# Optimization experiments

Hardware: AMD Instinct MI355X
Metric: run time of the kernel (lower is better)

## Reference

```python
import jax, jax.numpy as jnp
import numpy as np

N, E, C, NS, NB, NH = 20000, 320000, 64, 4, 8, 64
AVG_NEIGH = 16.0

def setup_inputs() -> dict:
    key = jax.random.key(0)
    ks = jax.random.split(key, 16)
    inp = {}
    inp['vectors'] = 0.35 * jax.random.normal(ks[0], (E, 3), jnp.float32)
    inp['node_scalars'] = jax.random.normal(ks[1], (N, C), jnp.float32)
    inp['node_vectors'] = jax.random.normal(ks[2], (N, C, 3), jnp.float32)
    inp['node_specie'] = jax.random.randint(ks[3], (N,), 0, NS)
    inp['senders'] = jax.random.randint(ks[4], (E,), 0, N)
    inp['receivers'] = jax.random.randint(ks[5], (E,), 0, N)
    # indexed skip linear: node irreps (64x0e+64x1o) -> 64x0e+64x1o+64x0e (scalars incl. gates)
    inp['W_skip_s'] = jax.random.normal(ks[6], (NS, C, 2 * C), jnp.float32) / np.sqrt(C)
    inp['W_skip_v'] = jax.random.normal(ks[7], (NS, C, C), jnp.float32) / np.sqrt(C)
    inp['W_up_s'] = jax.random.normal(ks[8], (C, C), jnp.float32) / np.sqrt(C)
    inp['W_up_v'] = jax.random.normal(ks[9], (C, C), jnp.float32) / np.sqrt(C)
    inp['W_mlp0'] = jax.random.normal(ks[10], (NB, NH), jnp.float32) / np.sqrt(NB)
    inp['W_mlp1'] = jax.random.normal(ks[11], (NH, NH), jnp.float32) / np.sqrt(NH)
    inp['W_mlp2'] = jax.random.normal(ks[12], (NH, 4 * C), jnp.float32) / np.sqrt(NH)
    inp['W_down_s'] = jax.random.normal(ks[13], (2 * C, 2 * C), jnp.float32) / np.sqrt(2 * C)
    inp['W_down_v'] = jax.random.normal(ks[14], (2 * C, C), jnp.float32) / np.sqrt(2 * C)
    return inp


def _forward(vectors, node_scalars, node_vectors, node_specie, senders, receivers,
             W_skip_s, W_skip_v, W_up_s, W_up_v, W_mlp0, W_mlp1, W_mlp2, W_down_s, W_down_v):
    n = node_scalars.shape[0]
    # --- self connection (specie-indexed linear) ---
    skip_s = jnp.einsum('ni,nio->no', node_scalars, W_skip_s[node_specie])   # [N,128]
    skip_v = jnp.einsum('nim,nio->nom', node_vectors, W_skip_v[node_specie]) # [N,64,3]
    # --- linear up ---
    s = node_scalars @ W_up_s                                  # [N,64]
    v = jnp.einsum('nim,io->nom', node_vectors, W_up_v)        # [N,64,3]
    ms, mv = s[senders], v[senders]                            # gather -> [E,64], [E,64,3]
    # --- spherical harmonics l=1, component normalization (|Y|=sqrt(3)) ---
    lengths = jnp.linalg.norm(vectors, axis=1, keepdims=True)  # [E,1]
    vhat = vectors / jnp.where(lengths == 0.0, 1.0, lengths)
    Y = jnp.sqrt(3.0) * vhat                                   # [E,3]
    # --- tensor product, filter_ir_out = {0e,1o} ---
    t1 = ms[:, :, None] * Y[:, None, :]                        # 0e x 1o -> 1o [E,64,3]
    t0 = jnp.einsum('ecm,em->ec', mv, Y) / jnp.sqrt(3.0)       # 1o x 1o -> 0e [E,64]
    msg_s = jnp.concatenate([ms, t0], axis=1)                  # [E,128]
    msg_v = jnp.concatenate([mv, t1], axis=1)                  # [E,128,3]
    # --- radial basis * polynomial envelope -> MLP ---
    x = lengths[:, 0]
    nvec = jnp.arange(1, NB + 1, dtype=vectors.dtype)
    safe_x = jnp.where(x == 0.0, 1.0, x)
    bess = jnp.sqrt(2.0) * jnp.sin(nvec * jnp.pi * x[:, None]) / safe_x[:, None]  # [E,8]
    u = jnp.clip(x, 0.0, 1.0)
    env = jnp.where(x < 1.0, 1.0 - 28.0 * u**6 + 48.0 * u**7 - 21.0 * u**8, 0.0)  # poly_envelope(5,2)
    h = jax.nn.swish((bess * env[:, None]) @ W_mlp0)
    h = jax.nn.swish(h @ W_mlp1)
    mix = h @ W_mlp2                                           # [E,256] = 128x0e + 128x1o weights
    mix = jnp.where(lengths == 0.0, 0.0, mix)
    msg_s = msg_s * mix[:, : 2 * C]
    msg_v = msg_v * mix[:, 2 * C :, None]
    # --- scatter-add to receivers, normalize by sqrt(avg_num_neighbors) ---
    inv = 1.0 / jnp.sqrt(AVG_NEIGH)
    agg_s = jnp.zeros((n, 2 * C), msg_s.dtype).at[receivers].add(msg_s) * inv
    agg_v = jnp.zeros((n, 2 * C, 3), msg_v.dtype).at[receivers].add(msg_v) * inv
    # --- linear down to 64x0e + 64x1o + 64x0e(gates) ---
    out_s = agg_s @ W_down_s + skip_s                          # [N,128]
    out_v = jnp.einsum('nim,io->nom', agg_v, W_down_v) + skip_v  # [N,64,3]
    # --- gate: swish on scalars, swish(gates) modulates vectors ---
    scal = jax.nn.swish(out_s[:, :C])
    gates = jax.nn.swish(out_s[:, C:])
    vec = out_v * gates[:, :, None]
    return jnp.concatenate([scal, vec.reshape(n, 3 * C)], axis=1)  # [N,256]


def reference(vectors, node_scalars, node_vectors, node_specie, senders, receivers,
              W_skip_s, W_skip_v, W_up_s, W_up_v, W_mlp0, W_mlp1, W_mlp2, W_down_s, W_down_v):
    return _forward(vectors, node_scalars, node_vectors, node_specie, senders, receivers,
                    W_skip_s, W_skip_v, W_up_s, W_up_v, W_mlp0, W_mlp1, W_mlp2, W_down_s, W_down_v)
```

## Files before the change

### kernel.cpp

```cpp
#include <hip/hip_runtime.h>
#include <math.h>

#define PI_F        3.14159265358979323846f
#define SQRT2_F     1.41421356237309515f
#define SQRT3_F     1.73205080756887729f
#define INV_SQRT3_F 0.57735026918962576f
#define INV_AVG     0.25f

#define N_NODES 20000
#define N_EDGES 320000

__device__ __forceinline__ float swish_f(float x) {
    return x / (1.f + __expf(-x));
}

__global__ __launch_bounds__(256) void k_zero_cnt(int* __restrict__ cnt) {
    const int i = blockIdx.x * 256 + threadIdx.x;
    if (i < N_NODES) cnt[i] = 0;
}
__global__ __launch_bounds__(256) void k_hist(const int* __restrict__ rcv,
                                              int* __restrict__ cnt) {
    const int e = blockIdx.x * 256 + threadIdx.x;
    if (e < N_EDGES) atomicAdd(&cnt[rcv[e]], 1);
}
__global__ __launch_bounds__(1024) void k_scan(const int* __restrict__ cnt,
                                               int* __restrict__ cursor) {
    __shared__ int part[1024];
    const int t = threadIdx.x;
    const int base = t * 20;
    int s = 0;
    #pragma unroll
    for (int j = 0; j < 20; ++j) {
        const int idx = base + j;
        if (idx < N_NODES) s += cnt[idx];
    }
    part[t] = s;
    __syncthreads();
    for (int d = 1; d < 1024; d <<= 1) {
        const int v = (t >= d) ? part[t - d] : 0;
        __syncthreads();
        part[t] += v;
        __syncthreads();
    }
    int run = (t == 0) ? 0 : part[t - 1];
    for (int j = 0; j < 20; ++j) {
        const int idx = base + j;
        if (idx < N_NODES) { cursor[idx] = run; run += cnt[idx]; }
    }
}
__global__ __launch_bounds__(256) void k_scatter(const int* __restrict__ rcv,
                                                 int* __restrict__ cursor,
                                                 int* __restrict__ perm) {
    const int e = blockIdx.x * 256 + threadIdx.x;
    if (e < N_EDGES) {
        const int pos = atomicAdd(&cursor[rcv[e]], 1);
        perm[pos] = e;
    }
}

__global__ __launch_bounds__(256) void k_node_up(
    const float* __restrict__ ns, const float* __restrict__ nv,
    const float* __restrict__ Wus, const float* __restrict__ Wuv,
    float* __restrict__ s_up, float* __restrict__ v_up,
    float* __restrict__ agg_s, float* __restrict__ agg_v)
{
    const int lane = threadIdx.x & 63;
    const int wq   = __builtin_amdgcn_readfirstlane(threadIdx.x >> 6);
    const int n    = blockIdx.x * 4 + wq;

    const float* nsr = ns + n * 64;
    const float* nvr = nv + n * 192;
    float acc = 0.f, a0 = 0.f, a1 = 0.f, a2 = 0.f;
    for (int i = 0; i < 64; ++i) {
        const float s = nsr[i];
        acc = fmaf(s, Wus[i*64 + lane], acc);
        const float wv = Wuv[i*64 + lane];
        a0 = fmaf(nvr[i*3+0], wv, a0);
        a1 = fmaf(nvr[i*3+1], wv, a1);
        a2 = fmaf(nvr[i*3+2], wv, a2);
    }
    s_up[n*64 + lane] = acc;
    v_up[(n*64 + lane)*3 + 0] = a0;
    v_up[(n*64 + lane)*3 + 1] = a1;
    v_up[(n*64 + lane)*3 + 2] = a2;

    agg_s[n*128 + lane]      = 0.f;
    agg_s[n*128 + 64 + lane] = 0.f;
    #pragma unroll
    for (int k = 0; k < 6; ++k) agg_v[n*384 + k*64 + lane] = 0.f;
}

__global__ __launch_bounds__(256, 4) void k_edge(
    const float* __restrict__ vecs,
    const int*   __restrict__ snd_idx, const int* __restrict__ rcv_idx,
    const int*   __restrict__ perm,
    const float* __restrict__ W0, const float* __restrict__ W1,
    const float* __restrict__ W2,
    const float* __restrict__ s_up, const float* __restrict__ v_up,
    float* __restrict__ agg_s, float* __restrict__ agg_v)
{
    __shared__ float h1v[64*69];
    __shared__ float h2v[64*69];

    const int tid  = threadIdx.x;
    const int lane = tid & 63;
    const int wq   = __builtin_amdgcn_readfirstlane(tid >> 6);
    const int e0   = blockIdx.x * 64;
    const int c    = lane & 15, q = lane >> 4;

    const int pe_l  = perm[e0 + lane];
    const int rcv_l = rcv_idx[pe_l];
    const int snd_l = snd_idx[pe_l];
    const float vx_l = vecs[pe_l*3+0], vy_l = vecs[pe_l*3+1], vz_l = vecs[pe_l*3+2];
    const float x_l  = sqrtf(vx_l*vx_l + vy_l*vy_l + vz_l*vz_l);
    const float sx_l = (x_l == 0.f) ? 1.f : x_l;
    const float ys_l = SQRT3_F / sx_l;
    const float Y0_l = vx_l * ys_l, Y1_l = vy_l * ys_l, Y2_l = vz_l * ys_l;
    const float msk_l = (x_l == 0.f) ? 0.f : 1.f;

    #pragma unroll 4
    for (int t = 0; t < 16; ++t) {
        const int le = wq*16 + t;
        const float x = __shfl(x_l, le);
        const float sx = (x == 0.f) ? 1.f : x;
        float s1, c1;
        __sincosf(PI_F * x, &s1, &c1);
        const float u  = fminf(x, 1.f);
        const float u2 = u*u, u3 = u2*u;
        const float u6 = u3*u3, u7 = u6*u, u8 = u6*u2;
        const float env  = (x < 1.f) ? (1.f - 28.f*u6 + 48.f*u7 - 21.f*u8) : 0.f;
        const float pref = SQRT2_F * env / sx;
        float h1 = 0.f;
        float sn = s1, snm1 = 0.f;
        const float twoc = 2.f * c1;
        #pragma unroll
        for (int b = 0; b < 8; ++b) {
            h1 = fmaf(pref * sn, W0[b*64 + lane], h1);
            const float snext = fmaf(twoc, sn, -snm1);
            snm1 = sn; sn = snext;
        }
        h1v[le*69 + lane] = swish_f(h1);
    }

    {
        float acc2[16];
        #pragma unroll
        for (int t = 0; t < 16; ++t) acc2[t] = 0.f;
        for (int i = 0; i < 64; ++i) {
            const float w = W1[i*64 + lane];
            #pragma unroll
            for (int t = 0; t < 16; ++t)
                acc2[t] = fmaf(h1v[(wq*16 + t)*69 + i], w, acc2[t]);
        }
        #pragma unroll
        for (int t = 0; t < 16; ++t)
            h2v[(wq*16 + t)*69 + lane] = swish_f(acc2[t]);
    }
    __syncthreads();

    float mixr[16][4];
    #pragma unroll
    for (int t = 0; t < 16; ++t)
        #pragma unroll
        for (int j = 0; j < 4; ++j) mixr[t][j] = 0.f;
    {
        const float* W2c = W2 + 64*wq + c;
        for (int i = 0; i < 64; ++i) {
            const float w0 = W2c[i*256 +  0];
            const float w1 = W2c[i*256 + 16];
            const float w2 = W2c[i*256 + 32];
            const float w3 = W2c[i*256 + 48];
            #pragma unroll
            for (int t = 0; t < 16; ++t) {
                const float h = h2v[(q*16 + t)*69 + i];
                mixr[t][0] = fmaf(h, w0, mixr[t][0]);
                mixr[t][1] = fmaf(h, w1, mixr[t][1]);
                mixr[t][2] = fmaf(h, w2, mixr[t][2]);
                mixr[t][3] = fmaf(h, w3, mixr[t][3]);
            }
        }
    }

    int cur = -1;
    if (wq == 0) {
        float ra0=0.f, ra1=0.f, ra2=0.f, ra3=0.f;
        #pragma unroll
        for (int t = 0; t < 16; ++t) {
            const int sl  = (lane & 48) + t;
            const int rcv = __shfl(rcv_l, sl);
            const int snd = __shfl(snd_l, sl);
            const float msk = __shfl(msk_l, sl);
            if (rcv != cur) {
                if (cur >= 0) {
                    float* p = agg_s + cur*128 + c;
                    unsafeAtomicAdd(p,      ra0);
                    unsafeAtomicAdd(p + 16, ra1);
                    unsafeAtomicAdd(p + 32, ra2);
                    unsafeAtomicAdd(p + 48, ra3);
                }
                ra0 = ra1 = ra2 = ra3 = 0.f; cur = rcv;
            }
            const float* sp = s_up + snd*64 + c;
            ra0 = fmaf(sp[0],  mixr[t][0] * msk, ra0);
            ra1 = fmaf(sp[16], mixr[t][1] * msk, ra1);
            ra2 = fmaf(sp[32], mixr[t][2] * msk, ra2);
            ra3 = fmaf(sp[48], mixr[t][3] * msk, ra3);
        }
        float* p = agg_s + cur*128 + c;
        unsafeAtomicAdd(p,      ra0);
        unsafeAtomicAdd(p + 16, ra1);
        unsafeAtomicAdd(p + 32, ra2);
        unsafeAtomicAdd(p + 48, ra3);
    } else if (wq == 1) {
        float ra0=0.f, ra1=0.f, ra2=0.f, ra3=0.f;
        #pragma unroll
        for (int t = 0; t < 16; ++t) {
            const int sl  = (lane & 48) + t;
            const int rcv = __shfl(rcv_l, sl);
            const int snd = __shfl(snd_l, sl);
            const float msk = __shfl(msk_l, sl);
            const float Y0 = __shfl(Y0_l, sl), Y1 = __shfl(Y1_l, sl), Y2 = __shfl(Y2_l, sl);
            if (rcv != cur) {
                if (cur >= 0) {
                    float* p = agg_s + cur*128 + 64 + c;
                    unsafeAtomicAdd(p,      ra0);
                    unsafeAtomicAdd(p + 16, ra1);
                    unsafeAtomicAdd(p + 32, ra2);
                    unsafeAtomicAdd(p + 48, ra3);
                }
                ra0 = ra1 = ra2 = ra3 = 0.f; cur = rcv;
            }
            const float* vp = v_up + (snd*64 + c)*3;
            const float t00 = (vp[  0]*Y0 + vp[  1]*Y1 + vp[  2]*Y2) * INV_SQRT3_F;
            const float t01 = (vp[ 48]*Y0 + vp[ 49]*Y1 + vp[ 50]*Y2) * INV_SQRT3_F;
            const float t02 = (vp[ 96]*Y0 + vp[ 97]*Y1 + vp[ 98]*Y2) * INV_SQRT3_F;
            const float t03 = (vp[144]*Y0 + vp[145]*Y1 + vp[146]*Y2) * INV_SQRT3_F;
            ra0 = fmaf(t00, mixr[t][0] * msk, ra0);
            ra1 = fmaf(t01, mixr[t][1] * msk, ra1);
            ra2 = fmaf(t02, mixr[t][2] * msk, ra2);
            ra3 = fmaf(t03, mixr[t][3] * msk, ra3);
        }
        float* p = agg_s + cur*128 + 64 + c;
        unsafeAtomicAdd(p,      ra0);
        unsafeAtomicAdd(p + 16, ra1);
        unsafeAtomicAdd(p + 32, ra2);
        unsafeAtomicAdd(p + 48, ra3);
    } else if (wq == 2) {
        float rv[4][3];
        #pragma unroll
        for (int i = 0; i < 4; ++i) { rv[i][0]=0.f; rv[i][1]=0.f; rv[i][2]=0.f; }
        #pragma unroll
        for (int t = 0; t < 16; ++t) {
            const int sl  = (lane & 48) + t;
            const int rcv = __shfl(rcv_l, sl);
            const int snd = __shfl(snd_l, sl);
            const float msk = __shfl(msk_l, sl);
            if (rcv != cur) {
                if (cur >= 0) {
                    float* p = agg_v + cur*384 + c*3;
                    #pragma unroll
                    for (int ntl = 0; ntl < 4; ++ntl)
                        #pragma unroll
                        for (int m = 0; m < 3; ++m)
                            unsafeAtomicAdd(p + ntl*48 + m, rv[ntl][m]);
                }
                #pragma unroll
                for (int i = 0; i < 4; ++i) { rv[i][0]=0.f; rv[i][1]=0.f; rv[i][2]=0.f; }
                cur = rcv;
            }
            const float* vp = v_up + (snd*64 + c)*3;
            #pragma unroll
            for (int ntl = 0; ntl < 4; ++ntl) {
                const float mx = mixr[t][ntl] * msk;
                #pragma unroll
                for (int m = 0; m < 3; ++m)
                    rv[ntl][m] = fmaf(vp[ntl*48 + m], mx, rv[ntl][m]);
            }
        }
        float* p = agg_v + cur*384 + c*3;
        #pragma unroll
        for (int ntl = 0; ntl < 4; ++ntl)
            #pragma unroll
            for (int m = 0; m < 3; ++m)
                unsafeAtomicAdd(p + ntl*48 + m, rv[ntl][m]);
    } else {
        float rv[4][3];
        #pragma unroll
        for (int i = 0; i < 4; ++i) { rv[i][0]=0.f; rv[i][1]=0.f; rv[i][2]=0.f; }
        #pragma unroll
        for (int t = 0; t < 16; ++t) {
            const int sl  = (lane & 48) + t;
            const int rcv = __shfl(rcv_l, sl);
            const int snd = __shfl(snd_l, sl);
            const float msk = __shfl(msk_l, sl);
            const float Y0 = __shfl(Y0_l, sl), Y1 = __shfl(Y1_l, sl), Y2 = __shfl(Y2_l, sl);
            if (rcv != cur) {
                if (cur >= 0) {
                    float* p = agg_v + cur*384 + 192 + c*3;
                    #pragma unroll
                    for (int ntl = 0; ntl < 4; ++ntl)
                        #pragma unroll
                        for (int m = 0; m < 3; ++m)
                            unsafeAtomicAdd(p + ntl*48 + m, rv[ntl][m]);
                }
                #pragma unroll
                for (int i = 0; i < 4; ++i) { rv[i][0]=0.f; rv[i][1]=0.f; rv[i][2]=0.f; }
                cur = rcv;
            }
            const float* sp = s_up + snd*64 + c;
            #pragma unroll
            for (int ntl = 0; ntl < 4; ++ntl) {
                const float mm = sp[ntl*16] * (mixr[t][ntl] * msk);
                rv[ntl][0] = fmaf(mm, Y0, rv[ntl][0]);
                rv[ntl][1] = fmaf(mm, Y1, rv[ntl][1]);
                rv[ntl][2] = fmaf(mm, Y2, rv[ntl][2]);
            }
        }
        float* p = agg_v + cur*384 + 192 + c*3;
        #pragma unroll
        for (int ntl = 0; ntl < 4; ++ntl)
            #pragma unroll
            for (int m = 0; m < 3; ++m)
                unsafeAtomicAdd(p + ntl*48 + m, rv[ntl][m]);
    }
}

__global__ __launch_bounds__(256) void k_node_down(
    const float* __restrict__ ns, const float* __restrict__ nv,
    const int*   __restrict__ spec_idx,
    const float* __restrict__ Wds, const float* __restrict__ Wdv,
    const float* __restrict__ Wsks, const float* __restrict__ Wskv,
    const float* __restrict__ agg_s, const float* __restrict__ agg_v,
    float* __restrict__ out)
{
    const int lane = threadIdx.x & 63;
    const int wq   = __builtin_amdgcn_readfirstlane(threadIdx.x >> 6);
    const int n    = blockIdx.x * 4 + wq;
    const int spec = __builtin_amdgcn_readfirstlane(spec_idx[n]);

    const float* ar  = agg_s + n*128;
    const float* avr = agg_v + n*384;
    float s0 = 0.f, s1 = 0.f, v0 = 0.f, v1 = 0.f, v2 = 0.f;
    for (int i = 0; i < 128; ++i) {
        const float a = ar[i] * INV_AVG;
        s0 = fmaf(a, Wds[i*128 + lane], s0);
        s1 = fmaf(a, Wds[i*128 + 64 + lane], s1);
        const float wv = Wdv[i*64 + lane];
        v0 = fmaf(avr[i*3+0] * INV_AVG, wv, v0);
        v1 = fmaf(avr[i*3+1] * INV_AVG, wv, v1);
        v2 = fmaf(avr[i*3+2] * INV_AVG, wv, v2);
    }
    const float* nsr = ns + n*64;
    const float* nvr = nv + n*192;
    const float* Ws  = Wsks + spec*8192;
    const float* Wv  = Wskv + spec*4096;
    for (int i = 0; i < 64; ++i) {
        const float s = nsr[i];
        s0 = fmaf(s, Ws[i*128 + lane], s0);
        s1 = fmaf(s, Ws[i*128 + 64 + lane], s1);
        const float wv = Wv[i*64 + lane];
        v0 = fmaf(nvr[i*3+0], wv, v0);
        v1 = fmaf(nvr[i*3+1], wv, v1);
        v2 = fmaf(nvr[i*3+2], wv, v2);
    }
    const float scal = swish_f(s0);
    const float gate = swish_f(s1);
    out[n*256 + lane]               = scal;
    out[n*256 + 64 + lane*3 + 0]    = v0 * gate;
    out[n*256 + 64 + lane*3 + 1]    = v1 * gate;
    out[n*256 + 64 + lane*3 + 2]    = v2 * gate;
}

extern "C" void kernel_launch(void* const* d_in, const int* in_sizes, int n_in,
                              void* d_out, int out_size, void* d_ws, size_t ws_size,
                              hipStream_t stream)
{
    (void)in_sizes; (void)n_in; (void)out_size; (void)ws_size;

    const float* vectors      = (const float*)d_in[0];
    const float* node_scalars = (const float*)d_in[1];
    const float* node_vectors = (const float*)d_in[2];
    const int*   node_specie  = (const int*)d_in[3];
    const int*   senders      = (const int*)d_in[4];
    const int*   receivers    = (const int*)d_in[5];
    const float* W_skip_s     = (const float*)d_in[6];
    const float* W_skip_v     = (const float*)d_in[7];
    const float* W_up_s       = (const float*)d_in[8];
    const float* W_up_v       = (const float*)d_in[9];
    const float* W_mlp0       = (const float*)d_in[10];
    const float* W_mlp1       = (const float*)d_in[11];
    const float* W_mlp2       = (const float*)d_in[12];
    const float* W_down_s     = (const float*)d_in[13];
    const float* W_down_v     = (const float*)d_in[14];
    float* out = (float*)d_out;

    float* ws    = (float*)d_ws;
    float* s_up  = ws;
    float* v_up  = s_up + 1280000;
    float* agg_s = v_up + 3840000;
    float* agg_v = agg_s + 2560000;
    int*   perm  = (int*)(agg_v + 7680000);
    int*   cnt    = (int*)agg_s;
    int*   cursor = cnt + 20000;

    hipLaunchKernelGGL(k_zero_cnt, dim3(79),   dim3(256),  0, stream, cnt);
    hipLaunchKernelGGL(k_hist,     dim3(1250), dim3(256),  0, stream, receivers, cnt);
    hipLaunchKernelGGL(k_scan,     dim3(1),    dim3(1024), 0, stream, cnt, cursor);
    hipLaunchKernelGGL(k_scatter,  dim3(1250), dim3(256),  0, stream, receivers, cursor, perm);

    hipLaunchKernelGGL(k_node_up, dim3(5000), dim3(256), 0, stream,
        node_scalars, node_vectors, W_up_s, W_up_v, s_up, v_up, agg_s, agg_v);
    hipLaunchKernelGGL(k_edge, dim3(5000), dim3(256), 0, stream,
        vectors, senders, receivers, perm, W_mlp0, W_mlp1, W_mlp2,
        s_up, v_up, agg_s, agg_v);
    hipLaunchKernelGGL(k_node_down, dim3(5000), dim3(256), 0, stream,
        node_scalars, node_vectors, node_specie, W_down_s, W_down_v,
        W_skip_s, W_skip_v, agg_s, agg_v, out);
}
```

Measured before the change: 543.1 us.

## Use fp16 MFMA for edge MLP output layer and batch node_down by species

Replaces the scalar FMA loop for the third edge-MLP layer (64->256) with fp16 MFMA 16x16x32 instructions, using a pre-packed fp16 copy of W_mlp2 and an fp16 LDS staging buffer for h2. Separately, nodes are bucketed by species (padded to multiples of 8) so each wavefront in k_node_down processes 8 nodes sharing one skip weight matrix, amortizing weight loads across nodes. This adds several small setup kernels and introduces fp16 rounding in the mix coefficients.

After: 1.003 ms. +84.6%, slower.

```diff
diff --git a/kernel.cpp b/kernel.cpp
--- a/kernel.cpp
+++ b/kernel.cpp
@@ -9,9 +9,28 @@
 
 #define N_NODES 20000
 #define N_EDGES 320000
+#define NPERM_SLOTS 20064
+
+typedef _Float16 f16x8 __attribute__((ext_vector_type(8)));
+typedef float    f32x4 __attribute__((ext_vector_type(4)));
+union HF8 { int4 i; f16x8 v; };
+union HF  { _Float16 h; unsigned short u; };
 
 __device__ __forceinline__ float swish_f(float x) {
     return x / (1.f + __expf(-x));
+}
+__device__ __forceinline__ unsigned short f2h(float f) {
+    HF x; x.h = (_Float16)f; return x.u;
+}
+
+__global__ __launch_bounds__(256) void k_prep_w(
+    const float* __restrict__ W2, unsigned short* __restrict__ W2p)
+{
+    const int t2 = blockIdx.x * 256 + threadIdx.x;
+    const int j = t2 & 7, l = (t2 >> 3) & 63, slot = t2 >> 9;
+    const int kt = slot >> 4, NT = slot & 15;
+    const int k = kt*32 + ((l >> 4) << 3) + j, n = NT*16 + (l & 15);
+    W2p[t2] = f2h(W2[k*256 + n]);
 }
 
 __global__ __launch_bounds__(256) void k_zero_cnt(int* __restrict__ cnt) {
@@ -58,6 +77,34 @@
     }
 }
 
+__global__ __launch_bounds__(256) void k_spec_init(int* __restrict__ nperm,
+                                                   int* __restrict__ scnt) {
+    const int i = blockIdx.x * 256 + threadIdx.x;
+    if (i < NPERM_SLOTS) nperm[i] = -1;
+    if (i < 4) scnt[i] = 0;
+}
+__global__ __launch_bounds__(256) void k_spec_hist(const int* __restrict__ spec,
+                                                   int* __restrict__ scnt) {
+    const int i = blockIdx.x * 256 + threadIdx.x;
+    if (i < N_NODES) atomicAdd(&scnt[spec[i]], 1);
+}
+__global__ __launch_bounds__(64) void k_spec_off(const int* __restrict__ scnt,
+                                                 int* __restrict__ scur) {
+    if (threadIdx.x == 0) {
+        int off = 0;
+        for (int s = 0; s < 4; ++s) { scur[s] = off; off += (scnt[s] + 7) & ~7; }
+    }
+}
+__global__ __launch_bounds__(256) void k_spec_scatter(const int* __restrict__ spec,
+                                                      int* __restrict__ scur,
+                                                      int* __restrict__ nperm) {
+    const int i = blockIdx.x * 256 + threadIdx.x;
+    if (i < N_NODES) {
+        const int pos = atomicAdd(&scur[spec[i]], 1);
+        nperm[pos] = i;
+    }
+}
+
 __global__ __launch_bounds__(256) void k_node_up(
     const float* __restrict__ ns, const float* __restrict__ nv,
     const float* __restrict__ Wus, const float* __restrict__ Wuv,
@@ -95,12 +142,12 @@
     const int*   __restrict__ snd_idx, const int* __restrict__ rcv_idx,
     const int*   __restrict__ perm,
     const float* __restrict__ W0, const float* __restrict__ W1,
-    const float* __restrict__ W2,
+    const unsigned short* __restrict__ W2p,
     const float* __restrict__ s_up, const float* __restrict__ v_up,
     float* __restrict__ agg_s, float* __restrict__ agg_v)
 {
     __shared__ float h1v[64*69];
-    __shared__ float h2v[64*69];
+    __shared__ __align__(16) unsigned short h2h[64*72];
 
     const int tid  = threadIdx.x;
     const int lane = tid & 63;
@@ -153,31 +200,28 @@
                 acc2[t] = fmaf(h1v[(wq*16 + t)*69 + i], w, acc2[t]);
         }
         #pragma unroll
-        for (int t = 0; t < 16; ++t)
-            h2v[(wq*16 + t)*69 + lane] = swish_f(acc2[t]);
+        for (int t = 0; t < 16; ++t) {
+            const int m = ((t & 12) << 2) + (wq << 2) + (t & 3);
+            h2h[m*72 + lane] = f2h(swish_f(acc2[t]));
+        }
     }
     __syncthreads();
 
-    float mixr[16][4];
+    const f32x4 z = {0.f, 0.f, 0.f, 0.f};
+    f32x4 accB[4][4] = {{z,z,z,z},{z,z,z,z},{z,z,z,z},{z,z,z,z}};
     #pragma unroll
-    for (int t = 0; t < 16; ++t)
-        #pragma unroll
-        for (int j = 0; j < 4; ++j) mixr[t][j] = 0.f;
-    {
-        const float* W2c = W2 + 64*wq + c;
-        for (int i = 0; i < 64; ++i) {
-            const float w0 = W2c[i*256 +  0];
-            const float w1 = W2c[i*256 + 16];
-            const float w2 = W2c[i*256 + 32];
-            const float w3 = W2c[i*256 + 48];
+    for (int kt = 0; kt < 2; ++kt) {
+        HF8 a[4];
+        #pragma unroll
+        for (int mt = 0; mt < 4; ++mt)
+            a[mt].i = *(const int4*)(h2h + (mt*16 + c)*72 + kt*32 + q*8);
+        #pragma unroll
+        for (int ntl = 0; ntl < 4; ++ntl) {
+            HF8 b;
+            b.i = *(const int4*)(W2p + ((kt*16 + 4*wq + ntl)*64 + lane)*8);
             #pragma unroll
-            for (int t = 0; t < 16; ++t) {
-                const float h = h2v[(q*16 + t)*69 + i];
-                mixr[t][0] = fmaf(h, w0, mixr[t][0]);
-                mixr[t][1] = fmaf(h, w1, mixr[t][1]);
-                mixr[t][2] = fmaf(h, w2, mixr[t][2]);
-                mixr[t][3] = fmaf(h, w3, mixr[t][3]);
-            }
+            for (int mt = 0; mt < 4; ++mt)
+                accB[mt][ntl] = __builtin_amdgcn_mfma_f32_16x16x32_f16(a[mt].v, b.v, accB[mt][ntl], 0, 0, 0);
         }
     }
 
@@ -200,11 +244,12 @@
                 }
                 ra0 = ra1 = ra2 = ra3 = 0.f; cur = rcv;
             }
+            const int mt = t >> 2, rr = t & 3;
             const float* sp = s_up + snd*64 + c;
-            ra0 = fmaf(sp[0],  mixr[t][0] * msk, ra0);
-            ra1 = fmaf(sp[16], mixr[t][1] * msk, ra1);
-            ra2 = fmaf(sp[32], mixr[t][2] * msk, ra2);
-            ra3 = fmaf(sp[48], mixr[t][3] * msk, ra3);
+            ra0 = fmaf(sp[0],  accB[mt][0][rr] * msk, ra0);
+            ra1 = fmaf(sp[16], accB[mt][1][rr] * msk, ra1);
+            ra2 = fmaf(sp[32], accB[mt][2][rr] * msk, ra2);
+            ra3 = fmaf(sp[48], accB[mt][3][rr] * msk, ra3);
         }
         float* p = agg_s + cur*128 + c;
         unsafeAtomicAdd(p,      ra0);
@@ -230,15 +275,16 @@
                 }
                 ra0 = ra1 = ra2 = ra3 = 0.f; cur = rcv;
             }
+            const int mt = t >> 2, rr = t & 3;
             const float* vp = v_up + (snd*64 + c)*3;
             const float t00 = (vp[  0]*Y0 + vp[  1]*Y1 + vp[  2]*Y2) * INV_SQRT3_F;
             const float t01 = (vp[ 48]*Y0 + vp[ 49]*Y1 + vp[ 50]*Y2) * INV_SQRT3_F;
             const float t02 = (vp[ 96]*Y0 + vp[ 97]*Y1 + vp[ 98]*Y2) * INV_SQRT3_F;
             const float t03 = (vp[144]*Y0 + vp[145]*Y1 + vp[146]*Y2) * INV_SQRT3_F;
-            ra0 = fmaf(t00, mixr[t][0] * msk, ra0);
-            ra1 = fmaf(t01, mixr[t][1] * msk, ra1);
-            ra2 = fmaf(t02, mixr[t][2] * msk, ra2);
-            ra3 = fmaf(t03, mixr[t][3] * msk, ra3);
+            ra0 = fmaf(t00, accB[mt][0][rr] * msk, ra0);
+            ra1 = fmaf(t01, accB[mt][1][rr] * msk, ra1);
+            ra2 = fmaf(t02, accB[mt][2][rr] * msk, ra2);
+            ra3 = fmaf(t03, accB[mt][3][rr] * msk, ra3);
         }
         float* p = agg_s + cur*128 + 64 + c;
         unsafeAtomicAdd(p,      ra0);
@@ -268,10 +314,11 @@
                 for (int i = 0; i < 4; ++i) { rv[i][0]=0.f; rv[i][1]=0.f; rv[i][2]=0.f; }
                 cur = rcv;
             }
+            const int mt = t >> 2, rr = t & 3;
             const float* vp = v_up + (snd*64 + c)*3;
             #pragma unroll
             for (int ntl = 0; ntl < 4; ++ntl) {
-                const float mx = mixr[t][ntl] * msk;
+                const float mx = accB[mt][ntl][rr] * msk;
                 #pragma unroll
                 for (int m = 0; m < 3; ++m)
                     rv[ntl][m] = fmaf(vp[ntl*48 + m], mx, rv[ntl][m]);
@@ -307,10 +354,11 @@
                 for (int i = 0; i < 4; ++i) { rv[i][0]=0.f; rv[i][1]=0.f; rv[i][2]=0.f; }
                 cur = rcv;
             }
+            const int mt = t >> 2, rr = t & 3;
             const float* sp = s_up + snd*64 + c;
             #pragma unroll
             for (int ntl = 0; ntl < 4; ++ntl) {
-                const float mm = sp[ntl*16] * (mixr[t][ntl] * msk);
+                const float mm = sp[ntl*16] * (accB[mt][ntl][rr] * msk);
                 rv[ntl][0] = fmaf(mm, Y0, rv[ntl][0]);
                 rv[ntl][1] = fmaf(mm, Y1, rv[ntl][1]);
                 rv[ntl][2] = fmaf(mm, Y2, rv[ntl][2]);
@@ -327,7 +375,7 @@
 
 __global__ __launch_bounds__(256) void k_node_down(
     const float* __restrict__ ns, const float* __restrict__ nv,
-    const int*   __restrict__ spec_idx,
+    const int*   __restrict__ spec_idx, const int* __restrict__ nperm,
     const float* __restrict__ Wds, const float* __restrict__ Wdv,
     const float* __restrict__ Wsks, const float* __restrict__ Wskv,
     const float* __restrict__ agg_s, const float* __restrict__ agg_v,
@@ -335,40 +383,68 @@
 {
     const int lane = threadIdx.x & 63;
     const int wq   = __builtin_amdgcn_readfirstlane(threadIdx.x >> 6);
-    const int n    = blockIdx.x * 4 + wq;
-    const int spec = __builtin_amdgcn_readfirstlane(spec_idx[n]);
-
-    const float* ar  = agg_s + n*128;
-    const float* avr = agg_v + n*384;
-    float s0 = 0.f, s1 = 0.f, v0 = 0.f, v1 = 0.f, v2 = 0.f;
+    const int base = blockIdx.x * 32 + wq * 8;
+
+    int nd[8];
+    #pragma unroll
+    for (int n = 0; n < 8; ++n) nd[n] = nperm[base + n];
+    if (nd[0] < 0) return;
+    const int spec = __builtin_amdgcn_readfirstlane(spec_idx[nd[0]]);
+
+    float s0[8], s1[8], v0[8], v1[8], v2[8];
+    #pragma unroll
+    for (int n = 0; n < 8; ++n) { s0[n]=0.f; s1[n]=0.f; v0[n]=0.f; v1[n]=0.f; v2[n]=0.f; }
+
+    #pragma unroll 2
     for (int i = 0; i < 128; ++i) {
-        const float a = ar[i] * INV_AVG;
-        s0 = fmaf(a, Wds[i*128 + lane], s0);
-        s1 = fmaf(a, Wds[i*128 + 64 + lane], s1);
+        const float w0 = Wds[i*128 + lane];
+        const float w1 = Wds[i*128 + 64 + lane];
         const float wv = Wdv[i*64 + lane];
-        v0 = fmaf(avr[i*3+0] * INV_AVG, wv, v0);
-        v1 = fmaf(avr[i*3+1] * INV_AVG, wv, v1);
-        v2 = fmaf(avr[i*3+2] * INV_AVG, wv, v2);
-    }
-    const float* nsr = ns + n*64;
-    const float* nvr = nv + n*192;
-    const float* Ws  = Wsks + spec*8192;
-    const float* Wv  = Wskv + spec*4096;
+        #pragma unroll
+        for (int n = 0; n < 8; ++n) {
+            if (nd[n] >= 0) {
+                const float a = agg_s[nd[n]*128 + i] * INV_AVG;
+                s0[n] = fmaf(a, w0, s0[n]);
+                s1[n] = fmaf(a, w1, s1[n]);
+                const float* avr = agg_v + nd[n]*384 + i*3;
+                v0[n] = fmaf(avr[0] * INV_AVG, wv, v0[n]);
+                v1[n] = fmaf(avr[1] * INV_AVG, wv, v1[n]);
+                v2[n] = fmaf(avr[2] * INV_AVG, wv, v2[n]);
+            }
+        }
+    }
+    const float* Ws = Wsks + spec*8192;
+    const float* Wv = Wskv + spec*4096;
+    #pragma unroll 2
     for (int i = 0; i < 64; ++i) {
-        const float s = nsr[i];
-        s0 = fmaf(s, Ws[i*128 + lane], s0);
-        s1 = fmaf(s, Ws[i*128 + 64 + lane], s1);
+        const float w0 = Ws[i*128 + lane];
+        const float w1 = Ws[i*128 + 64 + lane];
         const float wv = Wv[i*64 + lane];
-        v0 = fmaf(nvr[i*3+0], wv, v0);
-        v1 = fmaf(nvr[i*3+1], wv, v1);
-        v2 = fmaf(nvr[i*3+2], wv, v2);
-    }
-    const float scal = swish_f(s0);
-    const float gate = swish_f(s1);
-    out[n*256 + lane]               = scal;
-    out[n*256 + 64 + lane*3 + 0]    = v0 * gate;
-    out[n*256 + 64 + lane*3 + 1]    = v1 * gate;
-    out[n*256 + 64 + lane*3 + 2]    = v2 * gate;
+        #pragma unroll
+        for (int n = 0; n < 8; ++n) {
+            if (nd[n] >= 0) {
+                const float s = ns[nd[n]*64 + i];
+                s0[n] = fmaf(s, w0, s0[n]);
+                s1[n] = fmaf(s, w1, s1[n]);
+                const float* nvr = nv + nd[n]*192 + i*3;
+                v0[n] = fmaf(nvr[0], wv, v0[n]);
+                v1[n] = fmaf(nvr[1], wv, v1[n]);
+                v2[n] = fmaf(nvr[2], wv, v2[n]);
+            }
+        }
+    }
+    #pragma unroll
+    for (int n = 0; n < 8; ++n) {
+        if (nd[n] >= 0) {
+            const float scal = swish_f(s0[n]);
+            const float gate = swish_f(s1[n]);
+            float* orow = out + nd[n]*256;
+            orow[lane]            = scal;
+            orow[64 + lane*3 + 0] = v0[n] * gate;
+            orow[64 + lane*3 + 1] = v1[n] * gate;
+            orow[64 + lane*3 + 2] = v2[n] * gate;
+        }
+    }
 }
 
 extern "C" void kernel_launch(void* const* d_in, const int* in_sizes, int n_in,
@@ -400,8 +476,14 @@
     float* agg_s = v_up + 3840000;
     float* agg_v = agg_s + 2560000;
     int*   perm  = (int*)(agg_v + 7680000);
+    unsigned short* W2p = (unsigned short*)(perm + 320000);
+    int*   nperm = perm;
+    int*   scnt  = perm + NPERM_SLOTS;
+    int*   scur  = scnt + 4;
     int*   cnt    = (int*)agg_s;
     int*   cursor = cnt + 20000;
+
+    hipLaunchKernelGGL(k_prep_w, dim3(64), dim3(256), 0, stream, W_mlp2, W2p);
 
     hipLaunchKernelGGL(k_zero_cnt, dim3(79),   dim3(256),  0, stream, cnt);
     hipLaunchKernelGGL(k_hist,     dim3(1250), dim3(256),  0, stream, receivers, cnt);
@@ -411,9 +493,15 @@
     hipLaunchKernelGGL(k_node_up, dim3(5000), dim3(256), 0, stream,
         node_scalars, node_vectors, W_up_s, W_up_v, s_up, v_up, agg_s, agg_v);
     hipLaunchKernelGGL(k_edge, dim3(5000), dim3(256), 0, stream,
-        vectors, senders, receivers, perm, W_mlp0, W_mlp1, W_mlp2,
+        vectors, senders, receivers, perm, W_mlp0, W_mlp1, W2p,
         s_up, v_up, agg_s, agg_v);
-    hipLaunchKernelGGL(k_node_down, dim3(5000), dim3(256), 0, stream,
-        node_scalars, node_vectors, node_specie, W_down_s, W_down_v,
+
+    hipLaunchKernelGGL(k_spec_init,    dim3(80), dim3(256), 0, stream, nperm, scnt);
+    hipLaunchKernelGGL(k_spec_hist,    dim3(79), dim3(256), 0, stream, node_specie, scnt);
+    hipLaunchKernelGGL(k_spec_off,     dim3(1),  dim3(64),  0, stream, scnt, scur);
+    hipLaunchKernelGGL(k_spec_scatter, dim3(79), dim3(256), 0, stream, node_specie, scur, nperm);
+
+    hipLaunchKernelGGL(k_node_down, dim3(NPERM_SLOTS / 32), dim3(256), 0, stream,
+        node_scalars, node_vectors, node_specie, nperm, W_down_s, W_down_v,
         W_skip_s, W_skip_v, agg_s, agg_v, out);
 }
```
